# Kernel optimization log

Hardware: AMD Instinct MI355X
Metric: run time of the kernel (lower is better)

The kernel has to match this reference:

```python
import jax, jax.numpy as jnp
import numpy as np

MARGIN = 0.1
NUM_BINS = 1600  # FastAP histogram bins over squared-distance range [0, 4]


def _fastap_rewards(x, labels):
    """Per-query FastAP (Cakir et al.) with soft (triangular) histogram binning.
    x: [n, d] L2-normalized embeddings; labels: [n] int. Returns [n] rewards.
    Uses the fact that a triangular pulse of width delta spreads each distance
    over exactly two adjacent bins -> scatter-add instead of an [n,n,L] tensor."""
    n = x.shape[0]
    L = NUM_BINS + 1
    delta = 4.0 / NUM_BINS
    dist2 = jnp.clip(2.0 - 2.0 * (x @ x.T), 0.0, 4.0)  # [n, n]
    same = labels[:, None] == labels[None, :]
    eye = jnp.eye(n, dtype=bool)
    i_pos = same & ~eye
    i_neg = ~same

    t = dist2 / delta
    idx0 = jnp.clip(jnp.floor(t).astype(jnp.int32), 0, L - 1)
    idx1 = jnp.clip(idx0 + 1, 0, L - 1)
    frac = t - jnp.floor(t)
    rows = jnp.broadcast_to(jnp.arange(n)[:, None], (n, n))

    def hist(mask):
        m = mask.astype(x.dtype)
        h = jnp.zeros((n, L), x.dtype)
        h = h.at[rows, idx0].add((1.0 - frac) * m)
        h = h.at[rows, idx1].add(frac * m)
        return h

    h_pos = hist(i_pos)
    h_neg = hist(i_neg)
    H_pos = jnp.cumsum(h_pos, axis=1)
    H_all = jnp.cumsum(h_pos + h_neg, axis=1)
    n_pos = jnp.sum(i_pos, axis=1).astype(x.dtype)
    safe = H_all > 0
    ap = jnp.sum(jnp.where(safe, h_pos * H_pos / jnp.where(safe, H_all, 1.0), 0.0), axis=1)
    return jnp.where(n_pos > 0, ap / jnp.maximum(n_pos, 1.0), 0.0)


def _per_row_loss(inputs_col, targets_col, inputs_row, targets_row):
    """Vectorized form of compute_loss_list. Sorting in the original only serves
    to extract max pos / max neg similarity, so per-row maxima + masked sums
    reproduce the exact same math."""
    n = inputs_col.shape[0]
    sim = inputs_col @ inputs_row.T  # [n, m]
    pos = targets_col[:, None] == targets_row[None, :]
    neg = ~pos  # computed BEFORE removing the diagonal, as in the original
    eye = jnp.eye(n, dtype=bool)
    pos = pos.at[:, :n].set(pos[:, :n] & ~eye)

    has_pos = jnp.any(pos, axis=1)
    neg_max = jnp.max(jnp.where(neg, sim, -jnp.inf), axis=1)  # neg_pair_[-1]
    pos_max = jnp.max(jnp.where(pos, sim, -jnp.inf), axis=1)  # pos_pair_[-1]

    pos_sel = pos & (sim < (neg_max + MARGIN)[:, None])
    pos_loss = jnp.sum(jnp.where(pos_sel, 1.0 - sim, 0.0), axis=1)

    thr = jnp.maximum(0.6, pos_max) - MARGIN
    neg_sel = neg & (sim > thr[:, None])
    neg_loss = jnp.sum(jnp.where(neg_sel, sim, 0.0), axis=1)

    return jnp.where(has_pos, pos_loss + neg_loss, 0.0), n


def setup_inputs() -> dict:
    key = jax.random.key(0)
    k1, k2, k3, k4, k5 = jax.random.split(key, 5)
    n, m, d, ncls = 4096, 4096, 128, 512

    def unit(k, shape):
        v = jax.random.normal(k, shape, dtype=jnp.float32)
        return v / jnp.linalg.norm(v, axis=-1, keepdims=True)

    return {
        "inputs_col": unit(k1, (n, d)),
        "targets_col": jax.random.randint(k2, (n,), 0, ncls),
        "inputs_row": unit(k3, (m, d)),
        "targets_row": jax.random.randint(k4, (m,), 0, ncls),
        "reward_labels": jax.random.randint(k5, (n,), 0, ncls),
    }


def reference(inputs_col, targets_col, inputs_row, targets_row, reward_labels):
    loss_i, n = _per_row_loss(inputs_col, targets_col, inputs_row, targets_row)
    # torch.tensor(rewards) detaches rewards from the graph -> stop_gradient
    rewards = jax.lax.stop_gradient(_fastap_rewards(inputs_col, reward_labels))
    return jnp.sum(loss_i * (1.0 - rewards)) / n
```

## Files before the change

kernel.cpp:

```cpp
#include <hip/hip_runtime.h>


#define N_ROWS 4096
#define DIM 128
#define TILE 128
#define L_BINS 1601

typedef __bf16 bf16x8 __attribute__((ext_vector_type(8)));
typedef float f32x4 __attribute__((ext_vector_type(4)));

__device__ __forceinline__ unsigned short f32_to_bf16(float f) {
    unsigned int u = __float_as_uint(f);
    u = (u + 0x7FFFu + ((u >> 16) & 1u)) >> 16;
    return (unsigned short)u;
}

__device__ __forceinline__ float bf16_lo(unsigned int u) {
    return __uint_as_float(u << 16);
}
__device__ __forceinline__ float bf16_hi(unsigned int u) {
    return __uint_as_float(u & 0xFFFF0000u);
}

__device__ __forceinline__ void unpack8(uint4 pk, float* s) {
    s[0] = bf16_lo(pk.x); s[1] = bf16_hi(pk.x);
    s[2] = bf16_lo(pk.y); s[3] = bf16_hi(pk.y);
    s[4] = bf16_lo(pk.z); s[5] = bf16_hi(pk.z);
    s[6] = bf16_lo(pk.w); s[7] = bf16_hi(pk.w);
}

__device__ __forceinline__ void async_copy16(const void* g, void* l) {
    __builtin_amdgcn_global_load_lds(
        (const __attribute__((address_space(1))) unsigned int*)g,
        (__attribute__((address_space(3))) unsigned int*)l, 16, 0, 0);
}

__global__ __launch_bounds__(256) void cvt2_kernel(const float4* __restrict__ a,
                                                   const float4* __restrict__ b,
                                                   ushort4* __restrict__ oa,
                                                   ushort4* __restrict__ ob,
                                                   int nvec) {
    for (int idx = blockIdx.x * 256 + threadIdx.x; idx < 2 * nvec; idx += gridDim.x * 256) {
        bool second = idx >= nvec;
        int k = second ? idx - nvec : idx;
        float4 v = second ? b[k] : a[k];
        ushort4 o;
        o.x = f32_to_bf16(v.x); o.y = f32_to_bf16(v.y);
        o.z = f32_to_bf16(v.z); o.w = f32_to_bf16(v.w);
        if (second) ob[k] = o; else oa[k] = o;
    }
}

__global__ __launch_bounds__(256) void gemm_tile_kernel(const unsigned short* __restrict__ A,
                                                        const unsigned short* __restrict__ B0,
                                                        const unsigned short* __restrict__ B1,
                                                        unsigned short* __restrict__ C0,
                                                        unsigned short* __restrict__ C1,
                                                        int N) {
    __shared__ unsigned short As[TILE * DIM];
    __shared__ unsigned short Bs[TILE * DIM];
    int w = threadIdx.x >> 6;
    int lane = threadIdx.x & 63;
    int tm = blockIdx.y, tn = blockIdx.x;
    const unsigned short* B = blockIdx.z ? B1 : B0;
    unsigned short* C = blockIdx.z ? C1 : C0;

    const char* ga = (const char*)(A + (size_t)tm * TILE * DIM);
    const char* gb = (const char*)(B + (size_t)tn * TILE * DIM);
#pragma unroll
    for (int it = 0; it < 8; ++it) {
        int off = (w * 8 + it) * 1024;
        async_copy16(ga + off + lane * 16, (char*)As + off);
        async_copy16(gb + off + lane * 16, (char*)Bs + off);
    }
    __syncthreads();

    int wm = (w & 1) * 64;
    int wn = (w >> 1) * 64;
    int quad = lane >> 4;
    int l15 = lane & 15;

    f32x4 acc[4][4] = {};
#pragma unroll
    for (int kk = 0; kk < 4; ++kk) {
        int kb = kk * 32 + quad * 8;
        bf16x8 af[4], bfr[4];
#pragma unroll
        for (int mi = 0; mi < 4; ++mi)
            af[mi] = *(const bf16x8*)&As[(wm + mi * 16 + l15) * DIM + kb];
#pragma unroll
        for (int ni = 0; ni < 4; ++ni)
            bfr[ni] = *(const bf16x8*)&Bs[(wn + ni * 16 + l15) * DIM + kb];
#pragma unroll
        for (int mi = 0; mi < 4; ++mi)
#pragma unroll
            for (int ni = 0; ni < 4; ++ni)
                acc[mi][ni] = __builtin_amdgcn_mfma_f32_16x16x32_bf16(af[mi], bfr[ni], acc[mi][ni], 0, 0, 0);
    }

#pragma unroll
    for (int mi = 0; mi < 4; ++mi) {
        int row0 = tm * TILE + wm + mi * 16 + quad * 4;
#pragma unroll
        for (int ni = 0; ni < 4; ++ni) {
            int col = tn * TILE + wn + ni * 16 + l15;
#pragma unroll
            for (int r = 0; r < 4; ++r)
                C[(size_t)(row0 + r) * N + col] = f32_to_bf16(acc[mi][ni][r]);
        }
    }
}

__global__ __launch_bounds__(256) void lossap_kernel(const unsigned short* __restrict__ sim,
                                                     const unsigned short* __restrict__ gram,
                                                     const int* __restrict__ tcol,
                                                     const int* __restrict__ trow,
                                                     const int* __restrict__ rlab,
                                                     float* __restrict__ contrib,
                                                     int n) {
    __shared__ unsigned int histA[L_BINS];
    __shared__ unsigned int histP[L_BINS];
    __shared__ unsigned long long wsum[4];
    __shared__ float pmx[4], nmx[4], lsum[4], apw[4];
    __shared__ int npw[4];
    int i = blockIdx.x;
    int t = threadIdx.x;
    int w = t >> 6, lane = t & 63;

    for (int b = t; b < L_BINS; b += 256) { histA[b] = 0u; histP[b] = 0u; }

    int myt = tcol[i];
    int li = rlab[i];
    const uint4* simv = (const uint4*)(sim + (size_t)i * n);
    const uint4* grav = (const uint4*)(gram + (size_t)i * n);
    const int4* trv = (const int4*)trow;
    const int4* rlv = (const int4*)rlab;

    uint4 spk[2], gpk[2];
    int4 tl[4], rl[4];
#pragma unroll
    for (int vv = 0; vv < 2; ++vv) {
        int vi = vv * 256 + t;
        spk[vv] = simv[vi];
        gpk[vv] = grav[vi];
        tl[2 * vv] = trv[2 * vi];
        tl[2 * vv + 1] = trv[2 * vi + 1];
        rl[2 * vv] = rlv[2 * vi];
        rl[2 * vv + 1] = rlv[2 * vi + 1];
    }
    __syncthreads();

    float pmax = -3e38f, nmax = -3e38f;
    unsigned int posm = 0, negm = 0;
    int npos = 0;
#pragma unroll
    for (int vv = 0; vv < 2; ++vv) {
        int vi = vv * 256 + t;
        {
            float s[8];
            unpack8(spk[vv], s);
            int lab[8] = {tl[2 * vv].x, tl[2 * vv].y, tl[2 * vv].z, tl[2 * vv].w,
                          tl[2 * vv + 1].x, tl[2 * vv + 1].y, tl[2 * vv + 1].z, tl[2 * vv + 1].w};
#pragma unroll
            for (int k = 0; k < 8; ++k) {
                int j = vi * 8 + k;
                bool same = (lab[k] == myt);
                bool posf = same && (j != i);
                if (posf) pmax = fmaxf(pmax, s[k]);
                if (!same) nmax = fmaxf(nmax, s[k]);
                posm |= ((unsigned int)posf) << (vv * 8 + k);
                negm |= ((unsigned int)(!same)) << (vv * 8 + k);
            }
        }
        {
            float g[8];
            unpack8(gpk[vv], g);
            int lab[8] = {rl[2 * vv].x, rl[2 * vv].y, rl[2 * vv].z, rl[2 * vv].w,
                          rl[2 * vv + 1].x, rl[2 * vv + 1].y, rl[2 * vv + 1].z, rl[2 * vv + 1].w};
#pragma unroll
            for (int k = 0; k < 8; ++k) {
                int j = vi * 8 + k;
                float d2 = fminf(fmaxf(2.f - 2.f * g[k], 0.f), 4.f);
                float tt = d2 * 400.0f;
                float fl = floorf(tt);
                int i0 = (int)fl;
                if (i0 > L_BINS - 1) i0 = L_BINS - 1;
                int i1 = i0 + 1;
                if (i1 > L_BINS - 1) i1 = L_BINS - 1;
                unsigned int w1 = (unsigned int)((tt - fl) * 65536.0f);
                unsigned int w0 = 65536u - w1;
                bool diag = (j == i);
                if (diag) { w0 = 0u; w1 = 0u; }
                bool posf = (lab[k] == li) && !diag;
                atomicAdd(&histA[i0], w0);
                atomicAdd(&histA[i1], w1);
                if (posf) {
                    atomicAdd(&histP[i0], w0);
                    atomicAdd(&histP[i1], w1);
                    npos += 1;
                }
            }
        }
    }

#pragma unroll
    for (int off = 32; off > 0; off >>= 1) {
        pmax = fmaxf(pmax, __shfl_xor(pmax, off));
        nmax = fmaxf(nmax, __shfl_xor(nmax, off));
    }
    if (lane == 0) { pmx[w] = pmax; nmx[w] = nmax; }
    __syncthreads();

    pmax = fmaxf(fmaxf(pmx[0], pmx[1]), fmaxf(pmx[2], pmx[3]));
    nmax = fmaxf(fmaxf(nmx[0], nmx[1]), fmaxf(nmx[2], nmx[3]));

    float thr_n = nmax + 0.1f;
    float thr_p = fmaxf(0.6f, pmax) - 0.1f;
    float pl = 0.f, nl = 0.f;
#pragma unroll
    for (int vv = 0; vv < 2; ++vv) {
        float s[8];
        unpack8(spk[vv], s);
#pragma unroll
        for (int k = 0; k < 8; ++k) {
            int bit = vv * 8 + k;
            bool posf = (posm >> bit) & 1u;
            bool negf = (negm >> bit) & 1u;
            pl += (posf && s[k] < thr_n) ? 1.f - s[k] : 0.f;
            nl += (negf && s[k] > thr_p) ? s[k] : 0.f;
        }
    }
    float tot = pl + nl;
#pragma unroll
    for (int off = 32; off > 0; off >>= 1) tot += __shfl_xor(tot, off);

    const int CH = 7;
    int base = t * CH;
    unsigned long long lc[CH];
    unsigned long long run = 0ull;
#pragma unroll
    for (int k = 0; k < CH; ++k) {
        int idx = base + k;
        unsigned long long h = (idx < L_BINS)
            ? (((unsigned long long)histP[idx] << 32) | (unsigned long long)histA[idx])
            : 0ull;
        run += h;
        lc[k] = run;
    }
    unsigned long long tsum = run;
    unsigned long long sc = tsum;
#pragma unroll
    for (int off = 1; off < 64; off <<= 1) {
        unsigned long long v2 = __shfl_up(sc, off);
        if (lane >= off) sc += v2;
    }
    if (lane == 63) wsum[w] = sc;
    if (lane == 0) lsum[w] = tot;
    __syncthreads();
    unsigned long long woff = 0ull;
    for (int ww = 0; ww < w; ++ww) woff += wsum[ww];
    unsigned long long throff = woff + sc - tsum;

    float ap = 0.f;
#pragma unroll
    for (int k = 0; k < CH; ++k) {
        int idx = base + k;
        if (idx < L_BINS) {
            unsigned int hp = histP[idx];
            if (hp) {
                unsigned long long cum = lc[k] + throff;
                unsigned int Hp = (unsigned int)(cum >> 32);
                unsigned int Ha = (unsigned int)cum;
                ap += (float)hp * (float)Hp / (float)Ha;
            }
        }
    }
#pragma unroll
    for (int off = 32; off > 0; off >>= 1) {
        ap += __shfl_xor(ap, off);
        npos += __shfl_xor(npos, off);
    }
    if (lane == 0) { apw[w] = ap; npw[w] = npos; }
    __syncthreads();
    if (t == 0) {
        float loss_i = (pmax > -1e30f) ? (lsum[0] + lsum[1] + lsum[2] + lsum[3]) : 0.f;
        float A = apw[0] + apw[1] + apw[2] + apw[3];
        int np = npw[0] + npw[1] + npw[2] + npw[3];
        float reward = (np > 0) ? A * (1.0f / 65536.0f) / (float)np : 0.f;
        contrib[i] = loss_i * (1.f - reward);
    }
}

__global__ __launch_bounds__(256) void final_kernel(const float* __restrict__ contrib,
                                                    float* __restrict__ out, int n) {
    __shared__ float r[256];
    int t = threadIdx.x;
    float s = 0.f;
    for (int j = t; j < n; j += 256) s += contrib[j];
    r[t] = s;
    __syncthreads();
    for (int off = 128; off > 0; off >>= 1) {
        if (t < off) r[t] += r[t + off];
        __syncthreads();
    }
    if (t == 0) out[0] = r[0] / (float)n;
}

extern "C" void kernel_launch(void* const* d_in, const int* in_sizes, int n_in,
                              void* d_out, int out_size, void* d_ws, size_t ws_size,
                              hipStream_t stream) {
    const float* inputs_col = (const float*)d_in[0];
    const int* targets_col = (const int*)d_in[1];
    const float* inputs_row = (const float*)d_in[2];
    const int* targets_row = (const int*)d_in[3];
    const int* reward_labels = (const int*)d_in[4];
    float* out = (float*)d_out;

    const int n = N_ROWS, m = N_ROWS, d = DIM;
    char* ws = (char*)d_ws;
    const size_t MB = 1048576;
    unsigned short* simbuf = (unsigned short*)ws;
    unsigned short* grambuf = (unsigned short*)(ws + 32 * MB);
    unsigned short* Abf = (unsigned short*)(ws + 64 * MB);
    unsigned short* Rbf = (unsigned short*)(ws + 65 * MB);
    float* contrib = (float*)(ws + 66 * MB);

    cvt2_kernel<<<512, 256, 0, stream>>>((const float4*)inputs_col, (const float4*)inputs_row,
                                         (ushort4*)Abf, (ushort4*)Rbf, n * d / 4);

    dim3 ggrid(n / TILE, n / TILE, 2);
    gemm_tile_kernel<<<ggrid, 256, 0, stream>>>(Abf, Rbf, Abf, simbuf, grambuf, m);

    lossap_kernel<<<n, 256, 0, stream>>>(simbuf, grambuf, targets_col, targets_row,
                                         reward_labels, contrib, n);

    final_kernel<<<1, 256, 0, stream>>>(contrib, out, n);
}
```

Baseline: 125.3 us.

## Precompute label-match bitmasks in a separate kernel and remove diagonal via subtraction

Adds a mask_kernel that turns the label comparisons into packed byte bitmasks (pos-loss, neg-loss, pos-AP). The loss/AP kernel reads these in place of the per-row int4 label vectors, and each thread now handles 16 contiguous elements instead of two strided chunks. The diagonal is no longer masked inside the hot loop: it is added like any other element and then subtracted once with atomicSub. This cuts label loads and compares in the main kernel but adds a kernel launch and about 6 MB of mask writes and reads.

```diff
diff --git a/kernel.cpp b/kernel.cpp
--- a/kernel.cpp
+++ b/kernel.cpp
@@ -33,6 +33,40 @@
     __builtin_amdgcn_global_load_lds(
         (const __attribute__((address_space(1))) unsigned int*)g,
         (__attribute__((address_space(3))) unsigned int*)l, 16, 0, 0);
+}
+
+__global__ __launch_bounds__(256) void mask_kernel(const int* __restrict__ tcol,
+                                                   const int* __restrict__ trow,
+                                                   const int* __restrict__ rlab,
+                                                   unsigned char* __restrict__ PL,
+                                                   unsigned char* __restrict__ NL,
+                                                   unsigned char* __restrict__ PG) {
+    const int total = N_ROWS * (N_ROWS / 8);
+    const int4* trv = (const int4*)trow;
+    const int4* rlv = (const int4*)rlab;
+    for (int idx = blockIdx.x * 256 + threadIdx.x; idx < total; idx += gridDim.x * 256) {
+        int i = idx >> 9;
+        int b = idx & 511;
+        int j0 = b << 3;
+        int4 t0 = trv[b * 2], t1 = trv[b * 2 + 1];
+        int4 r0 = rlv[b * 2], r1 = rlv[b * 2 + 1];
+        int mt = tcol[i];
+        int mr = rlab[i];
+        int tj[8] = {t0.x, t0.y, t0.z, t0.w, t1.x, t1.y, t1.z, t1.w};
+        int rj[8] = {r0.x, r0.y, r0.z, r0.w, r1.x, r1.y, r1.z, r1.w};
+        unsigned int pl = 0, nl = 0, pg = 0;
+#pragma unroll
+        for (int k = 0; k < 8; ++k) {
+            int j = j0 + k;
+            bool sm = (tj[k] == mt);
+            pl |= ((unsigned int)(sm && j != i)) << k;
+            nl |= ((unsigned int)(!sm)) << k;
+            pg |= ((unsigned int)((rj[k] == mr) && j != i)) << k;
+        }
+        PL[idx] = (unsigned char)pl;
+        NL[idx] = (unsigned char)nl;
+        PG[idx] = (unsigned char)pg;
+    }
 }
 
 __global__ __launch_bounds__(256) void cvt2_kernel(const float4* __restrict__ a,
@@ -113,9 +147,9 @@
 
 __global__ __launch_bounds__(256) void lossap_kernel(const unsigned short* __restrict__ sim,
                                                      const unsigned short* __restrict__ gram,
-                                                     const int* __restrict__ tcol,
-                                                     const int* __restrict__ trow,
-                                                     const int* __restrict__ rlab,
+                                                     const unsigned char* __restrict__ PL,
+                                                     const unsigned char* __restrict__ NL,
+                                                     const unsigned char* __restrict__ PG,
                                                      float* __restrict__ contrib,
                                                      int n) {
     __shared__ unsigned int histA[L_BINS];
@@ -129,57 +163,39 @@
 
     for (int b = t; b < L_BINS; b += 256) { histA[b] = 0u; histP[b] = 0u; }
 
-    int myt = tcol[i];
-    int li = rlab[i];
     const uint4* simv = (const uint4*)(sim + (size_t)i * n);
     const uint4* grav = (const uint4*)(gram + (size_t)i * n);
-    const int4* trv = (const int4*)trow;
-    const int4* rlv = (const int4*)rlab;
 
     uint4 spk[2], gpk[2];
-    int4 tl[4], rl[4];
 #pragma unroll
     for (int vv = 0; vv < 2; ++vv) {
-        int vi = vv * 256 + t;
-        spk[vv] = simv[vi];
-        gpk[vv] = grav[vi];
-        tl[2 * vv] = trv[2 * vi];
-        tl[2 * vv + 1] = trv[2 * vi + 1];
-        rl[2 * vv] = rlv[2 * vi];
-        rl[2 * vv + 1] = rlv[2 * vi + 1];
-    }
+        spk[vv] = simv[2 * t + vv];
+        gpk[vv] = grav[2 * t + vv];
+    }
+    unsigned int pl16 = *(const unsigned short*)(PL + (size_t)i * 512 + 2 * t);
+    unsigned int nl16 = *(const unsigned short*)(NL + (size_t)i * 512 + 2 * t);
+    unsigned int pg16 = *(const unsigned short*)(PG + (size_t)i * 512 + 2 * t);
     __syncthreads();
 
     float pmax = -3e38f, nmax = -3e38f;
-    unsigned int posm = 0, negm = 0;
-    int npos = 0;
 #pragma unroll
     for (int vv = 0; vv < 2; ++vv) {
-        int vi = vv * 256 + t;
         {
             float s[8];
             unpack8(spk[vv], s);
-            int lab[8] = {tl[2 * vv].x, tl[2 * vv].y, tl[2 * vv].z, tl[2 * vv].w,
-                          tl[2 * vv + 1].x, tl[2 * vv + 1].y, tl[2 * vv + 1].z, tl[2 * vv + 1].w};
 #pragma unroll
             for (int k = 0; k < 8; ++k) {
-                int j = vi * 8 + k;
-                bool same = (lab[k] == myt);
-                bool posf = same && (j != i);
-                if (posf) pmax = fmaxf(pmax, s[k]);
-                if (!same) nmax = fmaxf(nmax, s[k]);
-                posm |= ((unsigned int)posf) << (vv * 8 + k);
-                negm |= ((unsigned int)(!same)) << (vv * 8 + k);
+                int e = vv * 8 + k;
+                if ((pl16 >> e) & 1u) pmax = fmaxf(pmax, s[k]);
+                if ((nl16 >> e) & 1u) nmax = fmaxf(nmax, s[k]);
             }
         }
         {
             float g[8];
             unpack8(gpk[vv], g);
-            int lab[8] = {rl[2 * vv].x, rl[2 * vv].y, rl[2 * vv].z, rl[2 * vv].w,
-                          rl[2 * vv + 1].x, rl[2 * vv + 1].y, rl[2 * vv + 1].z, rl[2 * vv + 1].w};
 #pragma unroll
             for (int k = 0; k < 8; ++k) {
-                int j = vi * 8 + k;
+                int e = vv * 8 + k;
                 float d2 = fminf(fmaxf(2.f - 2.f * g[k], 0.f), 4.f);
                 float tt = d2 * 400.0f;
                 float fl = floorf(tt);
@@ -189,18 +205,32 @@
                 if (i1 > L_BINS - 1) i1 = L_BINS - 1;
                 unsigned int w1 = (unsigned int)((tt - fl) * 65536.0f);
                 unsigned int w0 = 65536u - w1;
-                bool diag = (j == i);
-                if (diag) { w0 = 0u; w1 = 0u; }
-                bool posf = (lab[k] == li) && !diag;
                 atomicAdd(&histA[i0], w0);
                 atomicAdd(&histA[i1], w1);
-                if (posf) {
+                if ((pg16 >> e) & 1u) {
                     atomicAdd(&histP[i0], w0);
                     atomicAdd(&histP[i1], w1);
-                    npos += 1;
                 }
             }
         }
+    }
+    int npos = __popc(pg16);
+
+    if (t == (i >> 4)) {
+        int vv = (i >> 3) & 1, k = i & 7;
+        float g[8];
+        unpack8(gpk[vv], g);
+        float d2 = fminf(fmaxf(2.f - 2.f * g[k], 0.f), 4.f);
+        float tt = d2 * 400.0f;
+        float fl = floorf(tt);
+        int i0 = (int)fl;
+        if (i0 > L_BINS - 1) i0 = L_BINS - 1;
+        int i1 = i0 + 1;
+        if (i1 > L_BINS - 1) i1 = L_BINS - 1;
+        unsigned int w1 = (unsigned int)((tt - fl) * 65536.0f);
+        unsigned int w0 = 65536u - w1;
+        atomicSub(&histA[i0], w0);
+        atomicSub(&histA[i1], w1);
     }
 
 #pragma unroll
@@ -223,9 +253,9 @@
         unpack8(spk[vv], s);
 #pragma unroll
         for (int k = 0; k < 8; ++k) {
-            int bit = vv * 8 + k;
-            bool posf = (posm >> bit) & 1u;
-            bool negf = (negm >> bit) & 1u;
+            int e = vv * 8 + k;
+            bool posf = (pl16 >> e) & 1u;
+            bool negf = (nl16 >> e) & 1u;
             pl += (posf && s[k] < thr_n) ? 1.f - s[k] : 0.f;
             nl += (negf && s[k] > thr_p) ? s[k] : 0.f;
         }
@@ -324,6 +354,11 @@
     unsigned short* Abf = (unsigned short*)(ws + 64 * MB);
     unsigned short* Rbf = (unsigned short*)(ws + 65 * MB);
     float* contrib = (float*)(ws + 66 * MB);
+    unsigned char* PL = (unsigned char*)(ws + 67 * MB);
+    unsigned char* NL = (unsigned char*)(ws + 69 * MB);
+    unsigned char* PG = (unsigned char*)(ws + 71 * MB);
+
+    mask_kernel<<<2048, 256, 0, stream>>>(targets_col, targets_row, reward_labels, PL, NL, PG);
 
     cvt2_kernel<<<512, 256, 0, stream>>>((const float4*)inputs_col, (const float4*)inputs_row,
                                          (ushort4*)Abf, (ushort4*)Rbf, n * d / 4);
@@ -331,8 +366,7 @@
     dim3 ggrid(n / TILE, n / TILE, 2);
     gemm_tile_kernel<<<ggrid, 256, 0, stream>>>(Abf, Rbf, Abf, simbuf, grambuf, m);
 
-    lossap_kernel<<<n, 256, 0, stream>>>(simbuf, grambuf, targets_col, targets_row,
-                                         reward_labels, contrib, n);
+    lossap_kernel<<<n, 256, 0, stream>>>(simbuf, grambuf, PL, NL, PG, contrib, n);
 
     final_kernel<<<1, 256, 0, stream>>>(contrib, out, n);
 }
```

Result: slower. 133.1 us (+6.2%).
